# Performance work log

Hardware: AMD Instinct MI355X
Metric: run time of the kernel (lower is better)

The kernel has to match this reference:

```python
import jax, jax.numpy as jnp
import numpy as np

D = 2048
N = 16384
ETA = 0.01


def setup_inputs() -> dict:
    key = jax.random.key(0)
    k_theta, k_xs = jax.random.split(key)
    theta = jax.random.normal(k_theta, (D,), dtype=jnp.float32)
    # per-layer params x_k, init uniform(-1/sqrt(d), 1/sqrt(d)) as in torch module
    stdv = 1.0 / np.sqrt(D)
    xs = jax.random.uniform(k_xs, (N, D), dtype=jnp.float32, minval=-stdv, maxval=stdv)
    return {"theta": theta, "xs": xs}


def reference(theta, xs):
    # Each layer: pred = <x, theta>; grad = -x / (1 + exp(pred));
    # theta_next = theta - eta * grad = theta + eta * x / (1 + exp(pred)).
    def step(th, x):
        pred = jnp.dot(x, th)
        th_next = th + ETA * x / (1.0 + jnp.exp(pred))
        return th_next, None

    theta_out, _ = jax.lax.scan(step, theta, xs)
    return theta_out
```

## Files before the change

kernel.cpp:

```cpp
#include <hip/hip_runtime.h>
#include <hip/hip_bf16.h>
#include <stdint.h>

#define D_DIM 2048
#define N_STEPS 16384
#define B_BLK 1024
#define N_BLK (N_STEPS / B_BLK)
#define T_P (B_BLK / 128)
#define N_TILE (T_P * (T_P + 1) / 2)
#define ETA 0.01f
#define NWG 256
#define FLAG_STRIDE 16

typedef __attribute__((ext_vector_type(8))) short short8_t;
typedef __attribute__((ext_vector_type(4))) float floatx4;

__device__ __forceinline__ short f2bf(float f) {
  __hip_bfloat16 h = __float2bfloat16(f);
  return __builtin_bit_cast(short, h);
}
__device__ __forceinline__ float bf2f(uint32_t bits) {
  return __builtin_bit_cast(float, bits << 16);
}

__device__ __forceinline__ void store_wt(float* p, float v) {
  __hip_atomic_store(p, v, __ATOMIC_RELAXED, __HIP_MEMORY_SCOPE_AGENT);
}

__device__ __forceinline__ void gl_lds16(const short* g, short* l) {
  __builtin_amdgcn_global_load_lds(
      (const __attribute__((address_space(1))) void*)g,
      (__attribute__((address_space(3))) void*)l, 16, 0, 0);
}

__global__ __launch_bounds__(256) void cast_kernel(const float* __restrict__ xs,
                                                   short* __restrict__ xb) {
  size_t i = (size_t)blockIdx.x * 256 + threadIdx.x;
  float4 a = ((const float4*)xs)[i * 2];
  float4 b = ((const float4*)xs)[i * 2 + 1];
  short8_t v;
  v[0] = f2bf(a.x); v[1] = f2bf(a.y); v[2] = f2bf(a.z); v[3] = f2bf(a.w);
  v[4] = f2bf(b.x); v[5] = f2bf(b.y); v[6] = f2bf(b.z); v[7] = f2bf(b.w);
  *(short8_t*)(xb + i * 8) = v;
}

__global__ __launch_bounds__(256) void gram_kernel(const short* __restrict__ xb,
                                                   short* __restrict__ G) {
  int i = blockIdx.x;
  int x = i & 7, j = i >> 3;
  int b = (j < 36) ? x : x + 8;
  int t = (j < 36) ? j : j - 36;
  int ti = 0;
  while ((ti + 1) * (ti + 2) / 2 <= t) ti++;
  int tj = t - ti * (ti + 1) / 2;

  __shared__ short As[128 * 64];
  __shared__ short Bs[128 * 64];

  int tid = threadIdx.x;
  int lane = tid & 63;
  int w = tid >> 6;
  int wm = w >> 1, wn = w & 1;
  int quad = lane >> 4, rr = lane & 15;

  floatx4 acc[4][4];
#pragma unroll
  for (int ii = 0; ii < 4; ii++)
#pragma unroll
    for (int jj = 0; jj < 4; jj++)
#pragma unroll
      for (int r = 0; r < 4; r++) acc[ii][jj][r] = 0.f;

  const short* Arow = xb + (size_t)(b * B_BLK + ti * 128) * D_DIM;
  const short* Brow = xb + (size_t)(b * B_BLK + tj * 128) * D_DIM;
  bool diag = (ti == tj);

  for (int kk = 0; kk < D_DIM; kk += 64) {
#pragma unroll
    for (int tch = 0; tch < 4; tch++) {
      int chunk = tch * 256 + tid;
      int row = chunk >> 3, slot = chunk & 7;
      int cc = slot ^ (row & 7);
      gl_lds16(Arow + (size_t)row * D_DIM + kk + cc * 8, &As[chunk * 8]);
      if (!diag)
        gl_lds16(Brow + (size_t)row * D_DIM + kk + cc * 8, &Bs[chunk * 8]);
    }
    __syncthreads();

    const short* Bsrc = diag ? As : Bs;
#pragma unroll
    for (int ks = 0; ks < 2; ks++) {
      short8_t af[4], bfr[4];
#pragma unroll
      for (int mt = 0; mt < 4; mt++) {
        int r = wm * 64 + mt * 16 + rr;
        int slot = (ks * 4 + quad) ^ (r & 7);
        af[mt] = *(const short8_t*)(&As[r * 64 + slot * 8]);
      }
#pragma unroll
      for (int nt = 0; nt < 4; nt++) {
        int r = wn * 64 + nt * 16 + rr;
        int slot = (ks * 4 + quad) ^ (r & 7);
        bfr[nt] = *(const short8_t*)(&Bsrc[r * 64 + slot * 8]);
      }
#pragma unroll
      for (int mt = 0; mt < 4; mt++)
#pragma unroll
        for (int nt = 0; nt < 4; nt++)
          acc[mt][nt] = __builtin_amdgcn_mfma_f32_16x16x32_bf16(
              af[mt], bfr[nt], acc[mt][nt], 0, 0, 0);
    }
    __syncthreads();
  }

  size_t gbase = ((size_t)(b * N_TILE + t)) * (128 * 128);
  int col0 = lane & 15;
  int row0 = (lane >> 4) * 4;
#pragma unroll
  for (int mt = 0; mt < 4; mt++)
#pragma unroll
    for (int nt = 0; nt < 4; nt++)
#pragma unroll
      for (int r = 0; r < 4; r++) {
        int row = wm * 64 + mt * 16 + row0 + r;
        int col = wn * 64 + nt * 16 + col0;
        G[gbase + (size_t)row * 128 + col] = f2bf(acc[mt][nt][r]);
      }
}

__device__ __forceinline__ void bar_arrive(int* flags, int wg, int tid,
                                           int gen) {
  __syncthreads();
  if (tid == 0)
    __hip_atomic_store(&flags[wg * FLAG_STRIDE], gen, __ATOMIC_RELAXED,
                       __HIP_MEMORY_SCOPE_AGENT);
}

__device__ __forceinline__ void bar_wait(int* flags, int tid, int gen) {
  int guard = 0;
  while (__hip_atomic_load(&flags[tid * FLAG_STRIDE], __ATOMIC_RELAXED,
                           __HIP_MEMORY_SCOPE_AGENT) < gen &&
         guard < (1 << 20)) {
    guard++;
    __builtin_amdgcn_s_sleep(1);
  }
  asm volatile("" ::: "memory");
  __syncthreads();
}

__device__ __forceinline__ float wave_reduce(float s) {
  for (int off = 32; off; off >>= 1) s += __shfl_xor(s, off, 64);
  return s;
}

__global__ __launch_bounds__(256, 1) void solve_kernel(
    const short* __restrict__ xb, const short* __restrict__ G,
    float* __restrict__ theta_arr, float* __restrict__ c0_arr,
    float* __restrict__ c1_arr, int* flags, int* release) {
  int tid = threadIdx.x;
  int wg = blockIdx.x;
  int lane = tid & 63;
  int wid = tid >> 6;
  int gw = wg * 4 + wid;
  int ti = gw >> 7, kr = gw & 127;
  int oct = (wg & 7) * 32 + (wg >> 3);
  int d0 = oct * 8;
  int gen = 0;
  (void)release;

  __shared__ float redc[4][8];

  short8_t xa[4];
  uint32_t gv[8];
  short8_t xc[4];

  {
    const short* xr = xb + (size_t)gw * D_DIM;
#pragma unroll
    for (int i = 0; i < 4; i++)
      xa[i] = *(const short8_t*)(xr + (i * 64 + lane) * 8);
#pragma unroll
    for (int tj = 0; tj < T_P; tj++)
      if (tj <= ti) {
        size_t base = ((size_t)(ti * (ti + 1) / 2 + tj)) * (128 * 128) +
                      (size_t)kr * 128;
        gv[tj] = *(const uint32_t*)(G + base + lane * 2);
      }
  }

  for (int b = 0; b < N_BLK; b++) {
    const float* theta = theta_arr + (size_t)b * D_DIM;
    float* c0 = c0_arr + (size_t)b * B_BLK;
    float* c1 = c1_arr + (size_t)b * B_BLK;
    float p_k;
    float th8 = 0.f;

    {
      if (tid < 8) th8 = theta[d0 + tid];
      float s = 0.f;
#pragma unroll
      for (int i = 0; i < 4; i++) {
        int idx = (i * 64 + lane) * 8;
        float4 t0 = *(const float4*)(theta + idx);
        float4 t1 = *(const float4*)(theta + idx + 4);
        short8_t xv = xa[i];
        s += bf2f((uint16_t)xv[0]) * t0.x + bf2f((uint16_t)xv[1]) * t0.y +
             bf2f((uint16_t)xv[2]) * t0.z + bf2f((uint16_t)xv[3]) * t0.w +
             bf2f((uint16_t)xv[4]) * t1.x + bf2f((uint16_t)xv[5]) * t1.y +
             bf2f((uint16_t)xv[6]) * t1.z + bf2f((uint16_t)xv[7]) * t1.w;
      }
      s = wave_reduce(s);
      p_k = s;
      if (lane == 0) store_wt(&c0[gw], ETA / (1.f + __expf(s)));
    }
    bar_arrive(flags, wg, tid, ++gen);
    {
      const short* xp = xb + ((size_t)b * B_BLK + tid * 4) * D_DIM + d0;
#pragma unroll
      for (int j = 0; j < 4; j++)
        xc[j] = *(const short8_t*)(xp + (size_t)j * D_DIM);
    }
    bar_wait(flags, tid, gen);

    {
      float2 cv[T_P];
#pragma unroll
      for (int tj = 0; tj < T_P; tj++)
        if (tj <= ti) cv[tj] = *(const float2*)(c0 + tj * 128 + lane * 2);
      float s = 0.f;
      int jc = lane * 2;
#pragma unroll
      for (int tj = 0; tj < T_P; tj++)
        if (tj <= ti) {
          int lim = (tj == ti) ? kr : 128;
          if (jc < lim) s += bf2f(gv[tj] & 0xffffu) * cv[tj].x;
          if (jc + 1 < lim) s += bf2f(gv[tj] >> 16) * cv[tj].y;
        }
      s = wave_reduce(s);
      if (lane == 0) store_wt(&c1[gw], ETA / (1.f + __expf(p_k + s)));
    }
    bar_arrive(flags, wg, tid, ++gen);
    if (b + 1 < N_BLK) {
      const short* xr = xb + (size_t)((b + 1) * B_BLK + gw) * D_DIM;
#pragma unroll
      for (int i = 0; i < 4; i++)
        xa[i] = *(const short8_t*)(xr + (i * 64 + lane) * 8);
    }
    bar_wait(flags, tid, gen);

    {
      float4 c1v = *(const float4*)(c1 + tid * 4);
      float a8[8];
#pragma unroll
      for (int jj = 0; jj < 8; jj++) a8[jj] = 0.f;
#pragma unroll
      for (int j = 0; j < 4; j++) {
        float c = (&c1v.x)[j];
        short8_t xv = xc[j];
#pragma unroll
        for (int jj = 0; jj < 8; jj++) a8[jj] += c * bf2f((uint16_t)xv[jj]);
      }
#pragma unroll
      for (int off = 32; off; off >>= 1)
#pragma unroll
        for (int jj = 0; jj < 8; jj++) a8[jj] += __shfl_xor(a8[jj], off, 64);
      if (lane == 0) {
#pragma unroll
        for (int jj = 0; jj < 8; jj++) redc[wid][jj] = a8[jj];
      }
      __syncthreads();
      if (tid < 8) {
        float tot =
            redc[0][tid] + redc[1][tid] + redc[2][tid] + redc[3][tid];
        store_wt(&theta_arr[(size_t)(b + 1) * D_DIM + d0 + tid], th8 + tot);
      }
    }
    if (b + 1 < N_BLK) {
      bar_arrive(flags, wg, tid, ++gen);
      {
        size_t base =
            ((size_t)((b + 1) * N_TILE + ti * (ti + 1) / 2)) * (128 * 128) +
            (size_t)kr * 128;
#pragma unroll
        for (int tj = 0; tj < T_P; tj++)
          if (tj <= ti)
            gv[tj] = *(const uint32_t*)(G + base + (size_t)tj * (128 * 128) +
                                        lane * 2);
      }
      bar_wait(flags, tid, gen);
    }
  }
}

extern "C" void kernel_launch(void* const* d_in, const int* in_sizes, int n_in,
                              void* d_out, int out_size, void* d_ws,
                              size_t ws_size, hipStream_t stream) {
  const float* theta_in = (const float*)d_in[0];
  const float* xs = (const float*)d_in[1];

  char* ws = (char*)d_ws;
  const size_t XB_BYTES = (size_t)N_STEPS * D_DIM * sizeof(short);
  const size_t G_BYTES = (size_t)N_BLK * N_TILE * 128 * 128 * sizeof(short);
  short* xb = (short*)ws;
  short* G = (short*)(ws + XB_BYTES);
  float* theta_arr = (float*)(ws + XB_BYTES + G_BYTES);
  float* c0_arr = theta_arr + (size_t)(N_BLK + 1) * D_DIM;
  float* c1_arr = c0_arr + (size_t)N_BLK * B_BLK;
  int* flags = (int*)(c1_arr + (size_t)N_BLK * B_BLK);
  int* release = flags + NWG * FLAG_STRIDE;

  hipMemsetAsync(flags, 0, (NWG * FLAG_STRIDE + 16) * sizeof(int), stream);
  hipMemcpyAsync(theta_arr, theta_in, D_DIM * sizeof(float),
                 hipMemcpyDeviceToDevice, stream);

  cast_kernel<<<(N_STEPS * D_DIM / 8) / 256, 256, 0, stream>>>(xs, xb);
  gram_kernel<<<N_BLK * N_TILE, 256, 0, stream>>>(xb, G);
  solve_kernel<<<NWG, 256, 0, stream>>>(xb, G, theta_arr, c0_arr, c1_arr,
                                        flags, release);

  hipMemcpyAsync(d_out, theta_arr + (size_t)N_BLK * D_DIM,
                 D_DIM * sizeof(float), hipMemcpyDeviceToDevice, stream);
}
```

Measured before the change: 353.2 us.

## Replace flag-based grid barriers with poison-value dataflow polling on results

Removes the per-workgroup flag arrays and three-or-four global barriers per block. Consumers now poll the c0, c1 and theta values directly until they are no longer a 0xFFFFFFFF poison pattern written by a host-side memset, then stage theta and c0 in shared memory. The Gram tile loads move to the top of each block iteration, and the x-row loads are split into short4 chunks. This cuts barrier round trips and lets workgroups proceed as soon as their specific inputs are ready. The cost is more polled global traffic and a reliance on poison never matching a real float value.

```diff
diff --git a/kernel.cpp b/kernel.cpp
--- a/kernel.cpp
+++ b/kernel.cpp
@@ -10,9 +10,10 @@
 #define N_TILE (T_P * (T_P + 1) / 2)
 #define ETA 0.01f
 #define NWG 256
-#define FLAG_STRIDE 16
+#define POISON 0xFFFFFFFFu
 
 typedef __attribute__((ext_vector_type(8))) short short8_t;
+typedef __attribute__((ext_vector_type(4))) short short4_t;
 typedef __attribute__((ext_vector_type(4))) float floatx4;
 
 __device__ __forceinline__ short f2bf(float f) {
@@ -31,6 +32,49 @@
   __builtin_amdgcn_global_load_lds(
       (const __attribute__((address_space(1))) void*)g,
       (__attribute__((address_space(3))) void*)l, 16, 0, 0);
+}
+
+__device__ __forceinline__ void poll4(const float* p, float* out) {
+  const uint32_t* q = (const uint32_t*)p;
+  uint32_t v[4];
+  int guard = 0;
+  for (;;) {
+    bool ok = true;
+#pragma unroll
+    for (int j = 0; j < 4; j++)
+      v[j] = __hip_atomic_load(q + j, __ATOMIC_RELAXED,
+                               __HIP_MEMORY_SCOPE_AGENT);
+#pragma unroll
+    for (int j = 0; j < 4; j++) ok &= (v[j] != POISON);
+    if (ok || ++guard > (1 << 20)) break;
+    __builtin_amdgcn_s_sleep(1);
+  }
+#pragma unroll
+  for (int j = 0; j < 4; j++) out[j] = __builtin_bit_cast(float, v[j]);
+}
+
+__device__ __forceinline__ void poll8(const float* pa, const float* pb,
+                                      float* out) {
+  const uint32_t* a = (const uint32_t*)pa;
+  const uint32_t* b = (const uint32_t*)pb;
+  uint32_t v[8];
+  int guard = 0;
+  for (;;) {
+    bool ok = true;
+#pragma unroll
+    for (int j = 0; j < 4; j++) {
+      v[j] = __hip_atomic_load(a + j, __ATOMIC_RELAXED,
+                               __HIP_MEMORY_SCOPE_AGENT);
+      v[4 + j] = __hip_atomic_load(b + j, __ATOMIC_RELAXED,
+                                   __HIP_MEMORY_SCOPE_AGENT);
+    }
+#pragma unroll
+    for (int j = 0; j < 8; j++) ok &= (v[j] != POISON);
+    if (ok || ++guard > (1 << 20)) break;
+    __builtin_amdgcn_s_sleep(1);
+  }
+#pragma unroll
+  for (int j = 0; j < 8; j++) out[j] = __builtin_bit_cast(float, v[j]);
 }
 
 __global__ __launch_bounds__(256) void cast_kernel(const float* __restrict__ xs,
@@ -128,26 +172,6 @@
       }
 }
 
-__device__ __forceinline__ void bar_arrive(int* flags, int wg, int tid,
-                                           int gen) {
-  __syncthreads();
-  if (tid == 0)
-    __hip_atomic_store(&flags[wg * FLAG_STRIDE], gen, __ATOMIC_RELAXED,
-                       __HIP_MEMORY_SCOPE_AGENT);
-}
-
-__device__ __forceinline__ void bar_wait(int* flags, int tid, int gen) {
-  int guard = 0;
-  while (__hip_atomic_load(&flags[tid * FLAG_STRIDE], __ATOMIC_RELAXED,
-                           __HIP_MEMORY_SCOPE_AGENT) < gen &&
-         guard < (1 << 20)) {
-    guard++;
-    __builtin_amdgcn_s_sleep(1);
-  }
-  asm volatile("" ::: "memory");
-  __syncthreads();
-}
-
 __device__ __forceinline__ float wave_reduce(float s) {
   for (int off = 32; off; off >>= 1) s += __shfl_xor(s, off, 64);
   return s;
@@ -156,7 +180,7 @@
 __global__ __launch_bounds__(256, 1) void solve_kernel(
     const short* __restrict__ xb, const short* __restrict__ G,
     float* __restrict__ theta_arr, float* __restrict__ c0_arr,
-    float* __restrict__ c1_arr, int* flags, int* release) {
+    float* __restrict__ c1_arr) {
   int tid = threadIdx.x;
   int wg = blockIdx.x;
   int lane = tid & 63;
@@ -165,68 +189,82 @@
   int ti = gw >> 7, kr = gw & 127;
   int oct = (wg & 7) * 32 + (wg >> 3);
   int d0 = oct * 8;
-  int gen = 0;
-  (void)release;
-
+
+  __shared__ float theta_s[D_DIM];
+  __shared__ float c0s[B_BLK];
   __shared__ float redc[4][8];
 
-  short8_t xa[4];
+  short4_t xa[8];
+  short8_t xc[4];
   uint32_t gv[8];
-  short8_t xc[4];
 
   {
     const short* xr = xb + (size_t)gw * D_DIM;
 #pragma unroll
-    for (int i = 0; i < 4; i++)
-      xa[i] = *(const short8_t*)(xr + (i * 64 + lane) * 8);
-#pragma unroll
-    for (int tj = 0; tj < T_P; tj++)
-      if (tj <= ti) {
-        size_t base = ((size_t)(ti * (ti + 1) / 2 + tj)) * (128 * 128) +
-                      (size_t)kr * 128;
-        gv[tj] = *(const uint32_t*)(G + base + lane * 2);
-      }
+    for (int i = 0; i < 8; i++)
+      xa[i] = *(const short4_t*)(xr + (i * 64 + lane) * 4);
   }
 
   for (int b = 0; b < N_BLK; b++) {
-    const float* theta = theta_arr + (size_t)b * D_DIM;
+    const float* theta_g = theta_arr + (size_t)b * D_DIM;
     float* c0 = c0_arr + (size_t)b * B_BLK;
     float* c1 = c1_arr + (size_t)b * B_BLK;
+
+    {
+      size_t base = ((size_t)(b * N_TILE + ti * (ti + 1) / 2)) * (128 * 128) +
+                    (size_t)kr * 128;
+#pragma unroll
+      for (int tj = 0; tj < T_P; tj++)
+        if (tj <= ti)
+          gv[tj] = *(const uint32_t*)(G + base + (size_t)tj * (128 * 128) +
+                                      lane * 2);
+    }
+    asm volatile("" ::: "memory");
+
+    {
+      float tv[8];
+      poll8(theta_g + tid * 4, theta_g + 1024 + tid * 4, tv);
+      *(float4*)(theta_s + tid * 4) = *(const float4*)(tv);
+      *(float4*)(theta_s + 1024 + tid * 4) = *(const float4*)(tv + 4);
+    }
+    __syncthreads();
+    float th8 = (tid < 8) ? theta_s[d0 + tid] : 0.f;
+
     float p_k;
-    float th8 = 0.f;
-
-    {
-      if (tid < 8) th8 = theta[d0 + tid];
+    {
       float s = 0.f;
 #pragma unroll
-      for (int i = 0; i < 4; i++) {
-        int idx = (i * 64 + lane) * 8;
-        float4 t0 = *(const float4*)(theta + idx);
-        float4 t1 = *(const float4*)(theta + idx + 4);
-        short8_t xv = xa[i];
+      for (int i = 0; i < 8; i++) {
+        float4 t0 = *(const float4*)(theta_s + (i * 64 + lane) * 4);
+        short4_t xv = xa[i];
         s += bf2f((uint16_t)xv[0]) * t0.x + bf2f((uint16_t)xv[1]) * t0.y +
-             bf2f((uint16_t)xv[2]) * t0.z + bf2f((uint16_t)xv[3]) * t0.w +
-             bf2f((uint16_t)xv[4]) * t1.x + bf2f((uint16_t)xv[5]) * t1.y +
-             bf2f((uint16_t)xv[6]) * t1.z + bf2f((uint16_t)xv[7]) * t1.w;
+             bf2f((uint16_t)xv[2]) * t0.z + bf2f((uint16_t)xv[3]) * t0.w;
       }
       s = wave_reduce(s);
       p_k = s;
       if (lane == 0) store_wt(&c0[gw], ETA / (1.f + __expf(s)));
     }
-    bar_arrive(flags, wg, tid, ++gen);
+
     {
       const short* xp = xb + ((size_t)b * B_BLK + tid * 4) * D_DIM + d0;
 #pragma unroll
       for (int j = 0; j < 4; j++)
         xc[j] = *(const short8_t*)(xp + (size_t)j * D_DIM);
     }
-    bar_wait(flags, tid, gen);
+    asm volatile("" ::: "memory");
+
+    {
+      float cv4[4];
+      poll4(c0 + tid * 4, cv4);
+      *(float4*)(c0s + tid * 4) = *(const float4*)(cv4);
+    }
+    __syncthreads();
 
     {
       float2 cv[T_P];
 #pragma unroll
       for (int tj = 0; tj < T_P; tj++)
-        if (tj <= ti) cv[tj] = *(const float2*)(c0 + tj * 128 + lane * 2);
+        if (tj <= ti) cv[tj] = *(const float2*)(c0s + tj * 128 + lane * 2);
       float s = 0.f;
       int jc = lane * 2;
 #pragma unroll
@@ -239,23 +277,24 @@
       s = wave_reduce(s);
       if (lane == 0) store_wt(&c1[gw], ETA / (1.f + __expf(p_k + s)));
     }
-    bar_arrive(flags, wg, tid, ++gen);
+
     if (b + 1 < N_BLK) {
       const short* xr = xb + (size_t)((b + 1) * B_BLK + gw) * D_DIM;
 #pragma unroll
-      for (int i = 0; i < 4; i++)
-        xa[i] = *(const short8_t*)(xr + (i * 64 + lane) * 8);
-    }
-    bar_wait(flags, tid, gen);
-
-    {
-      float4 c1v = *(const float4*)(c1 + tid * 4);
+      for (int i = 0; i < 8; i++)
+        xa[i] = *(const short4_t*)(xr + (i * 64 + lane) * 4);
+    }
+    asm volatile("" ::: "memory");
+
+    {
+      float c1v[4];
+      poll4(c1 + tid * 4, c1v);
       float a8[8];
 #pragma unroll
       for (int jj = 0; jj < 8; jj++) a8[jj] = 0.f;
 #pragma unroll
       for (int j = 0; j < 4; j++) {
-        float c = (&c1v.x)[j];
+        float c = c1v[j];
         short8_t xv = xc[j];
 #pragma unroll
         for (int jj = 0; jj < 8; jj++) a8[jj] += c * bf2f((uint16_t)xv[jj]);
@@ -274,20 +313,6 @@
             redc[0][tid] + redc[1][tid] + redc[2][tid] + redc[3][tid];
         store_wt(&theta_arr[(size_t)(b + 1) * D_DIM + d0 + tid], th8 + tot);
       }
-    }
-    if (b + 1 < N_BLK) {
-      bar_arrive(flags, wg, tid, ++gen);
-      {
-        size_t base =
-            ((size_t)((b + 1) * N_TILE + ti * (ti + 1) / 2)) * (128 * 128) +
-            (size_t)kr * 128;
-#pragma unroll
-        for (int tj = 0; tj < T_P; tj++)
-          if (tj <= ti)
-            gv[tj] = *(const uint32_t*)(G + base + (size_t)tj * (128 * 128) +
-                                        lane * 2);
-      }
-      bar_wait(flags, tid, gen);
     }
   }
 }
@@ -306,17 +331,16 @@
   float* theta_arr = (float*)(ws + XB_BYTES + G_BYTES);
   float* c0_arr = theta_arr + (size_t)(N_BLK + 1) * D_DIM;
   float* c1_arr = c0_arr + (size_t)N_BLK * B_BLK;
-  int* flags = (int*)(c1_arr + (size_t)N_BLK * B_BLK);
-  int* release = flags + NWG * FLAG_STRIDE;
-
-  hipMemsetAsync(flags, 0, (NWG * FLAG_STRIDE + 16) * sizeof(int), stream);
+
+  hipMemsetAsync(theta_arr + D_DIM, 0xFF,
+                 (size_t)(N_BLK * D_DIM + 2 * N_BLK * B_BLK) * sizeof(float),
+                 stream);
   hipMemcpyAsync(theta_arr, theta_in, D_DIM * sizeof(float),
                  hipMemcpyDeviceToDevice, stream);
 
   cast_kernel<<<(N_STEPS * D_DIM / 8) / 256, 256, 0, stream>>>(xs, xb);
   gram_kernel<<<N_BLK * N_TILE, 256, 0, stream>>>(xb, G);
-  solve_kernel<<<NWG, 256, 0, stream>>>(xb, G, theta_arr, c0_arr, c1_arr,
-                                        flags, release);
+  solve_kernel<<<NWG, 256, 0, stream>>>(xb, G, theta_arr, c0_arr, c1_arr);
 
   hipMemcpyAsync(d_out, theta_arr + (size_t)N_BLK * D_DIM,
                  D_DIM * sizeof(float), hipMemcpyDeviceToDevice, stream);
```

Result: slower. 386.3 us (+9.4%).
